# Kernel optimization log

Measured on AMD Instinct MI355X. Metric: run time of the kernel, lower is better.

The kernel has to match this reference:

```python
import jax, jax.numpy as jnp
import numpy as np

D = 1024      # n_embd
NH = 16       # attention heads
E = 8         # n_experts
K = 2         # k_best
FF = 4 * D    # expert MLP hidden
EPS = 1e-6    # rms_norm_epsilon
TEMP = 1.0    # target_temperature


def setup_inputs() -> dict:
    key = jax.random.key(0)
    ks = jax.random.split(key, 12)
    B, S = 2, 1024
    s = 0.02
    return {
        "x": jax.random.normal(ks[0], (B, S, D), jnp.float32),
        "attn_norm_w": jnp.ones((D,), jnp.float32),
        "wq": jax.random.normal(ks[1], (D, D), jnp.float32) * s,
        "wk": jax.random.normal(ks[2], (D, D), jnp.float32) * s,
        "wv": jax.random.normal(ks[3], (D, D), jnp.float32) * s,
        "wo": jax.random.normal(ks[4], (D, D), jnp.float32) * s,
        "mlp_norm_w": jnp.ones((D,), jnp.float32),
        "router_w": jax.random.normal(ks[5], (D, E), jnp.float32) * s,
        "w1": jax.random.normal(ks[6], (E, D, FF), jnp.float32) * s,
        "b1": jnp.zeros((E, FF), jnp.float32),
        "w2": jax.random.normal(ks[7], (E, FF, D), jnp.float32) * s,
        "b2": jnp.zeros((E, D), jnp.float32),
    }


def _rmsnorm(x, w):
    var = jnp.mean(jnp.square(x), axis=-1, keepdims=True)
    return x * jax.lax.rsqrt(var + EPS) * w


def _attention(x, wq, wk, wv, wo):
    B, S, _ = x.shape
    dh = D // NH
    q = (x @ wq).reshape(B, S, NH, dh)
    k = (x @ wk).reshape(B, S, NH, dh)
    v = (x @ wv).reshape(B, S, NH, dh)
    scores = jnp.einsum("bqhd,bkhd->bhqk", q, k) / jnp.sqrt(jnp.float32(dh))
    causal = jnp.tril(jnp.ones((S, S), bool))  # [S,S]
    scores = jnp.where(causal[None, None], scores, jnp.finfo(scores.dtype).min)
    attn = jax.nn.softmax(scores, axis=-1)
    out = jnp.einsum("bhqk,bkhd->bqhd", attn, v).reshape(B, S, D)
    return out @ wo


def reference(x, attn_norm_w, wq, wk, wv, wo, mlp_norm_w, router_w, w1, b1, w2, b2):
    B, S, _ = x.shape
    # attention sub-block
    x = x + _attention(_rmsnorm(x, attn_norm_w), wq, wk, wv, wo)
    residual = x
    h = _rmsnorm(x, mlp_norm_w)  # [B,S,D]

    # router: temperature softmax + top-k
    logits = h @ router_w / TEMP                      # [B,S,E]
    probs = jax.nn.softmax(logits, axis=-1)
    top_k_scores, top_k_indices = jax.lax.top_k(probs, K)  # [B,S,K]
    onehot = jax.nn.one_hot(top_k_indices, E, dtype=h.dtype)  # [B,S,K,E]
    gates = jnp.einsum("bsk,bske->bse", top_k_scores, onehot)  # [B,S,E]

    # load-balancing loss (Switch-style) + expert counts
    counts = jnp.sum(onehot, axis=(0, 1, 2))          # [E]
    frac = counts / (B * S * K)
    mean_prob = jnp.mean(probs, axis=(0, 1))          # [E]
    balancing_loss = E * jnp.sum(frac * mean_prob)

    # experts: dense dispatch; tokens with zero gate contribute nothing,
    # so this matches the sort/gather/scatter top-k combine exactly.
    pre = jnp.einsum("bsd,edf->ebsf", h, w1) + b1[:, None, None]  # [E,B,S,FF]
    act = jax.nn.gelu(pre)
    y = jnp.einsum("ebsf,efd->ebsd", act, w2) + b2[:, None, None]  # [E,B,S,D]
    moe = jnp.einsum("ebsd,bse->bsd", y, gates)

    out = residual + moe
    return out, balancing_loss, counts
```

## Files before the change

kernel.cpp:

```cpp
#include <hip/hip_runtime.h>

typedef __bf16 bf16;
typedef __bf16 bf16x4 __attribute__((ext_vector_type(4)));
typedef __bf16 bf16x8 __attribute__((ext_vector_type(8)));
typedef float f32x4 __attribute__((ext_vector_type(4)));

#define D_   1024
#define S_   1024
#define B_   2
#define NTOK 2048
#define FF_  4096
#define NE   8
#define CAP  5120
#define OUTN 2097152

__device__ __forceinline__ float gelu_f(float x) {
    float u = 0.7978845608028654f * (x + 0.044715f * x * x * x);
    float a = fabsf(u);
    float e = __expf(-2.0f * a);
    float t = (1.0f - e) / (1.0f + e);
    t = copysignf(t, u);
    return 0.5f * x * (1.0f + t);
}

__device__ __forceinline__ void gload16(const void* g, void* l) {
    __builtin_amdgcn_global_load_lds((const __attribute__((address_space(1))) unsigned int*)g,
                                     (__attribute__((address_space(3))) unsigned int*)l,
                                     16, 0, 0);
}

#define VMCNT(n) asm volatile("s_waitcnt vmcnt(" n ")" ::: "memory")
#define BARRIER() do { asm volatile("" ::: "memory"); \
                       __builtin_amdgcn_s_barrier();  \
                       asm volatile("" ::: "memory"); } while (0)

__global__ __launch_bounds__(256) void rmsnorm_k(const float* __restrict__ x,
                                                 const float* __restrict__ w,
                                                 float* __restrict__ yf,
                                                 bf16* __restrict__ yhi,
                                                 bf16* __restrict__ ylo) {
    int row = blockIdx.x;
    int t = threadIdx.x;
    const float* xr = x + (size_t)row * D_;
    float4 v = *(const float4*)(xr + t * 4);
    float ss = v.x * v.x + v.y * v.y + v.z * v.z + v.w * v.w;
    for (int off = 32; off; off >>= 1) ss += __shfl_down(ss, off);
    __shared__ float wsum[4];
    if ((t & 63) == 0) wsum[t >> 6] = ss;
    __syncthreads();
    float tot = wsum[0] + wsum[1] + wsum[2] + wsum[3];
    float rr = rsqrtf(tot * (1.0f / D_) + 1e-6f);
    float4 wv = *(const float4*)(w + t * 4);
    float y[4];
    y[0] = v.x * rr * wv.x; y[1] = v.y * rr * wv.y;
    y[2] = v.z * rr * wv.z; y[3] = v.w * rr * wv.w;
    if (yf) *(float4*)(yf + (size_t)row * D_ + t * 4) = *(float4*)y;
    if (yhi) {
#pragma unroll
        for (int i = 0; i < 4; i++) {
            bf16 hi = (bf16)y[i];
            yhi[(size_t)row * D_ + t * 4 + i] = hi;
            if (ylo) ylo[(size_t)row * D_ + t * 4 + i] = (bf16)(y[i] - (float)hi);
        }
    }
}

__global__ __launch_bounds__(256) void trans_split_k(
    const float* __restrict__ w0, const float* __restrict__ w1p,
    const float* __restrict__ w2p, const float* __restrict__ w3,
    bf16* o0h, bf16* o0l, bf16* o1h, bf16* o1l,
    bf16* o2h, bf16* o2l, bf16* o3h, bf16* o3l) {
    int z = blockIdx.z;
    const float* src = (z == 0) ? w0 : (z == 1) ? w1p : (z == 2) ? w2p : w3;
    bf16* dh = (z == 0) ? o0h : (z == 1) ? o1h : (z == 2) ? o2h : o3h;
    bf16* dl = (z == 0) ? o0l : (z == 1) ? o1l : (z == 2) ? o2l : o3l;
    __shared__ float tl[32][33];
    int c0 = blockIdx.x * 32, r0 = blockIdx.y * 32;
    int tx = threadIdx.x & 31, ty = threadIdx.x >> 5;
#pragma unroll
    for (int i = 0; i < 4; i++) {
        int r = ty + i * 8;
        tl[r][tx] = src[(size_t)(r0 + r) * 1024 + c0 + tx];
    }
    __syncthreads();
#pragma unroll
    for (int i = 0; i < 4; i++) {
        int c = ty + i * 8;
        float v = tl[tx][c];
        bf16 hi = (bf16)v;
        dh[(size_t)(c0 + c) * 1024 + r0 + tx] = hi;
        dl[(size_t)(c0 + c) * 1024 + r0 + tx] = (bf16)(v - (float)hi);
    }
}

__global__ __launch_bounds__(256) void transpose_cast4_k(const float* __restrict__ in,
                                                         bf16* __restrict__ out,
                                                         int R, int C) {
    __shared__ float tl[64][65];
    size_t base = (size_t)blockIdx.z * R * C;
    const float* src = in + base;
    bf16* dst = out + base;
    int c0 = blockIdx.x * 64, r0 = blockIdx.y * 64;
    int t = threadIdx.x;
    int lr = t >> 4;
    int lc = (t & 15) * 4;
#pragma unroll
    for (int i = 0; i < 4; i++) {
        int r = lr + i * 16;
        float4 v = *(const float4*)(src + (size_t)(r0 + r) * C + c0 + lc);
        tl[r][lc] = v.x; tl[r][lc + 1] = v.y; tl[r][lc + 2] = v.z; tl[r][lc + 3] = v.w;
    }
    __syncthreads();
    int wc = t >> 4;
    int wr = (t & 15) * 4;
#pragma unroll
    for (int i = 0; i < 4; i++) {
        int c = wc + i * 16;
        bf16x4 o;
        o[0] = (bf16)tl[wr][c];     o[1] = (bf16)tl[wr + 1][c];
        o[2] = (bf16)tl[wr + 2][c]; o[3] = (bf16)tl[wr + 3][c];
        *(bf16x4*)(dst + (size_t)(c0 + c) * R + r0 + wr) = o;
    }
}

__global__ __launch_bounds__(256) void vtrans_k(const bf16* __restrict__ vh,
                                                const bf16* __restrict__ vl,
                                                bf16* __restrict__ vth,
                                                bf16* __restrict__ vtl) {
    int s0 = blockIdx.x * 64;
    int bh = blockIdx.y;
    int b = bh >> 4, h = bh & 15;
    const bf16* src = blockIdx.z ? vl : vh;
    bf16* dst = blockIdx.z ? vtl : vth;
    __shared__ bf16 tl[64][65];
    int t = threadIdx.x;
    int lr = t >> 4, lc = (t & 15) * 4;
#pragma unroll
    for (int i = 0; i < 4; i++) {
        int r = lr + i * 16;
        bf16x4 v = *(const bf16x4*)(src + (size_t)(b * S_ + s0 + r) * D_ + h * 64 + lc);
        tl[r][lc] = v[0]; tl[r][lc + 1] = v[1]; tl[r][lc + 2] = v[2]; tl[r][lc + 3] = v[3];
    }
    __syncthreads();
    int wc = t >> 4, wr = (t & 15) * 4;
#pragma unroll
    for (int i = 0; i < 4; i++) {
        int c = wc + i * 16;
        bf16x4 o;
        o[0] = tl[wr][c];     o[1] = tl[wr + 1][c];
        o[2] = tl[wr + 2][c]; o[3] = tl[wr + 3][c];
        *(bf16x4*)(dst + (size_t)(bh * 64 + c) * S_ + s0 + wr) = o;
    }
}

#define SPLIT_STAGE(bi, k0)                             \
    gload16(gah0 + (k0), Lah[bi] + wv * 512);           \
    gload16(gah1 + (k0), Lah[bi] + 2048 + wv * 512);    \
    gload16(gal0 + (k0), Lal[bi] + wv * 512);           \
    gload16(gal1 + (k0), Lal[bi] + 2048 + wv * 512);    \
    gload16(gbh0 + (k0), Lbh[bi] + wv * 512);           \
    gload16(gbh1 + (k0), Lbh[bi] + 2048 + wv * 512);    \
    gload16(gbl0 + (k0), Lbl[bi] + wv * 512);           \
    gload16(gbl1 + (k0), Lbl[bi] + 2048 + wv * 512);

#define SPLIT_COMPUTE(bi) {                                                            \
    bf16x8 fah[4], fal[4], fbh[4], fbl[4];                                             \
    _Pragma("unroll") for (int i = 0; i < 4; i++) {                                    \
        fah[i] = *(const bf16x8*)(Lah[bi] + ra_off[i]);                                \
        fal[i] = *(const bf16x8*)(Lal[bi] + ra_off[i]);                                \
        fbh[i] = *(const bf16x8*)(Lbh[bi] + rb_off[i]);                                \
        fbl[i] = *(const bf16x8*)(Lbl[bi] + rb_off[i]);                                \
    }                                                                                  \
    _Pragma("unroll") for (int mt = 0; mt < 4; mt++)                                   \
    _Pragma("unroll") for (int nt = 0; nt < 4; nt++) {                                 \
        acc[mt][nt] = __builtin_amdgcn_mfma_f32_16x16x32_bf16(fah[mt], fbh[nt], acc[mt][nt], 0, 0, 0); \
        acc[mt][nt] = __builtin_amdgcn_mfma_f32_16x16x32_bf16(fah[mt], fbl[nt], acc[mt][nt], 0, 0, 0); \
        acc[mt][nt] = __builtin_amdgcn_mfma_f32_16x16x32_bf16(fal[mt], fbh[nt], acc[mt][nt], 0, 0, 0); \
    } }

#define SPLIT_STEP(bi, VM)          \
    VMCNT(VM);                      \
    BARRIER();                      \
    SPLIT_COMPUTE(bi);              \
    BARRIER();

#define SPLIT_DECLS(KOFF)                                                              \
    __shared__ __align__(16) bf16 Lah[2][4096];                                        \
    __shared__ __align__(16) bf16 Lal[2][4096];                                        \
    __shared__ __align__(16) bf16 Lbh[2][4096];                                        \
    __shared__ __align__(16) bf16 Lbl[2][4096];                                        \
    int t = threadIdx.x;                                                               \
    int wv = t >> 6, ln = t & 63;                                                      \
    int wm = wv >> 1, wn = wv & 1, l15 = ln & 15, qd = ln >> 4;                        \
    int sr0 = t >> 2, sr1 = 64 + sr0, cl = t & 3;                                      \
    int cs0 = (cl ^ ((sr0 >> 1) & 3)) * 8;                                             \
    int cs1 = (cl ^ ((sr1 >> 1) & 3)) * 8;                                             \
    const bf16* gah0 = Ah + (size_t)(m0 + sr0) * 1024 + (KOFF) + cs0;                  \
    const bf16* gah1 = Ah + (size_t)(m0 + sr1) * 1024 + (KOFF) + cs1;                  \
    const bf16* gal0 = Al + (size_t)(m0 + sr0) * 1024 + (KOFF) + cs0;                  \
    const bf16* gal1 = Al + (size_t)(m0 + sr1) * 1024 + (KOFF) + cs1;                  \
    const bf16* gbh0 = Bh + (size_t)(n0 + sr0) * 1024 + (KOFF) + cs0;                  \
    const bf16* gbh1 = Bh + (size_t)(n0 + sr1) * 1024 + (KOFF) + cs1;                  \
    const bf16* gbl0 = Bl + (size_t)(n0 + sr0) * 1024 + (KOFF) + cs0;                  \
    const bf16* gbl1 = Bl + (size_t)(n0 + sr1) * 1024 + (KOFF) + cs1;                  \
    int ra_off[4], rb_off[4];                                                          \
    _Pragma("unroll") for (int i = 0; i < 4; i++) {                                    \
        int r1 = wm * 64 + i * 16 + l15;                                               \
        ra_off[i] = r1 * 32 + (qd ^ ((r1 >> 1) & 3)) * 8;                              \
        int r2 = wn * 64 + i * 16 + l15;                                               \
        rb_off[i] = r2 * 32 + (qd ^ ((r2 >> 1) & 3)) * 8;                              \
    }                                                                                  \
    f32x4 acc[4][4];                                                                   \
    _Pragma("unroll") for (int mt = 0; mt < 4; mt++)                                   \
    _Pragma("unroll") for (int nt = 0; nt < 4; nt++) acc[mt][nt] = (f32x4){0.f,0.f,0.f,0.f};

__global__ __launch_bounds__(256) void gemm_qkv_k(
    const bf16* __restrict__ Ah, const bf16* __restrict__ Al,
    const bf16* __restrict__ Bqh, const bf16* __restrict__ Bql,
    const bf16* __restrict__ Bkh, const bf16* __restrict__ Bkl,
    const bf16* __restrict__ Bvh, const bf16* __restrict__ Bvl,
    bf16* Cqh, bf16* Cql, bf16* Ckh, bf16* Ckl, bf16* Cvh, bf16* Cvl) {
    int gy = blockIdx.y, zw = gy >> 3;
    const bf16* Bh = (zw == 0) ? Bqh : (zw == 1) ? Bkh : Bvh;
    const bf16* Bl = (zw == 0) ? Bql : (zw == 1) ? Bkl : Bvl;
    bf16* Ch = (zw == 0) ? Cqh : (zw == 1) ? Ckh : Cvh;
    bf16* Cl = (zw == 0) ? Cql : (zw == 1) ? Ckl : Cvl;
    int m0 = blockIdx.x * 128, n0 = (gy & 7) * 128;
    SPLIT_DECLS(0)
    SPLIT_STAGE(0, 0);
    for (int k0 = 0; k0 < 960; k0 += 64) {
        SPLIT_STAGE(1, k0 + 32);
        SPLIT_STEP(0, "8");
        SPLIT_STAGE(0, k0 + 64);
        SPLIT_STEP(1, "8");
    }
    SPLIT_STAGE(1, 992);
    SPLIT_STEP(0, "8");
    SPLIT_STEP(1, "0");
#pragma unroll
    for (int mt = 0; mt < 4; mt++)
#pragma unroll
        for (int nt = 0; nt < 4; nt++)
#pragma unroll
            for (int r = 0; r < 4; r++) {
                int gm = m0 + wm * 64 + mt * 16 + qd * 4 + r;
                int gn = n0 + wn * 64 + nt * 16 + l15;
                float vv = acc[mt][nt][r];
                bf16 hi = (bf16)vv;
                Ch[(size_t)gm * D_ + gn] = hi;
                Cl[(size_t)gm * D_ + gn] = (bf16)(vv - (float)hi);
            }
}

__global__ __launch_bounds__(256) void gemm_wo_k(
    const bf16* __restrict__ Ah, const bf16* __restrict__ Al,
    const bf16* __restrict__ Bh, const bf16* __restrict__ Bl,
    float* __restrict__ C) {
    int m0 = blockIdx.x * 128, n0 = blockIdx.y * 128;
    int kb = blockIdx.z * 256;
    SPLIT_DECLS(kb)
    SPLIT_STAGE(0, 0);
    for (int k0 = 0; k0 < 192; k0 += 64) {
        SPLIT_STAGE(1, k0 + 32);
        SPLIT_STEP(0, "8");
        SPLIT_STAGE(0, k0 + 64);
        SPLIT_STEP(1, "8");
    }
    SPLIT_STAGE(1, 224);
    SPLIT_STEP(0, "8");
    SPLIT_STEP(1, "0");
#pragma unroll
    for (int mt = 0; mt < 4; mt++)
#pragma unroll
        for (int nt = 0; nt < 4; nt++)
#pragma unroll
            for (int r = 0; r < 4; r++) {
                int gm = m0 + wm * 64 + mt * 16 + qd * 4 + r;
                int gn = n0 + wn * 64 + nt * 16 + l15;
                atomicAdd(&C[(size_t)gm * D_ + gn], acc[mt][nt][r]);
            }
}

#define AP 72

__global__ __launch_bounds__(256) void attn_mfma_k(
    const bf16* __restrict__ qhp, const bf16* __restrict__ qlp,
    const bf16* __restrict__ khp, const bf16* __restrict__ klp,
    const bf16* __restrict__ vth, const bf16* __restrict__ vtl,
    bf16* __restrict__ aoh, bf16* __restrict__ aol) {
    int qt = (int)gridDim.x - 1 - (int)blockIdx.x;
    int h = blockIdx.y, b = blockIdx.z;
    __shared__ __align__(16) bf16 Ksh[4096], Ksl[4096], VTh[4096], VTl[4096];
    __shared__ bf16 Ph[4][16 * AP], Pl[4][16 * AP];
    int t = threadIdx.x, wv = t >> 6, ln = t & 63, l15 = ln & 15, qd = ln >> 4;

    bf16x8 aqh[2], aql[2];
    {
        size_t qb = ((size_t)(b * S_ + qt * 64 + wv * 16 + l15)) * D_ + h * 64 + qd * 8;
        aqh[0] = *(const bf16x8*)(qhp + qb);
        aqh[1] = *(const bf16x8*)(qhp + qb + 32);
        aql[0] = *(const bf16x8*)(qlp + qb);
        aql[1] = *(const bf16x8*)(qlp + qb + 32);
    }

    int srow = t >> 3, scl = t & 7;
    int gsc = (scl ^ (srow & 7)) * 8;
    const bf16* kh0 = khp + (size_t)(b * S_ + srow) * D_ + h * 64 + gsc;
    const bf16* kh1 = khp + (size_t)(b * S_ + srow + 32) * D_ + h * 64 + gsc;
    const bf16* kl0 = klp + (size_t)(b * S_ + srow) * D_ + h * 64 + gsc;
    const bf16* kl1 = klp + (size_t)(b * S_ + srow + 32) * D_ + h * 64 + gsc;
    const bf16* vt0 = vth + (size_t)((b * 16 + h) * 64 + srow) * S_ + gsc;
    const bf16* vt1 = vth + (size_t)((b * 16 + h) * 64 + srow + 32) * S_ + gsc;
    const bf16* wl0 = vtl + (size_t)((b * 16 + h) * 64 + srow) * S_ + gsc;
    const bf16* wl1 = vtl + (size_t)((b * 16 + h) * 64 + srow + 32) * S_ + gsc;

    int soff[4][2];
#pragma unroll
    for (int nt = 0; nt < 4; nt++)
#pragma unroll
        for (int ks = 0; ks < 2; ks++) {
            int r = nt * 16 + l15;
            soff[nt][ks] = r * 64 + ((ks * 4 + qd) ^ (r & 7)) * 8;
        }

    f32x4 oacc[4];
    float mrow[4], lrow[4];
#pragma unroll
    for (int i = 0; i < 4; i++) {
        oacc[i] = (f32x4){0.f, 0.f, 0.f, 0.f};
        mrow[i] = -1e30f; lrow[i] = 0.0f;
    }

    for (int kt = 0; kt <= qt; kt++) {
        BARRIER();
        size_t ko = (size_t)kt * 64 * D_;
        int vo = kt * 64;
        gload16(kh0 + ko, Ksh + wv * 512); gload16(kh1 + ko, Ksh + 2048 + wv * 512);
        gload16(kl0 + ko, Ksl + wv * 512); gload16(kl1 + ko, Ksl + 2048 + wv * 512);
        gload16(vt0 + vo, VTh + wv * 512); gload16(vt1 + vo, VTh + 2048 + wv * 512);
        gload16(wl0 + vo, VTl + wv * 512); gload16(wl1 + vo, VTl + 2048 + wv * 512);
        VMCNT("0");
        BARRIER();

        f32x4 sacc[4];
#pragma unroll
        for (int nt = 0; nt < 4; nt++) sacc[nt] = (f32x4){0.f, 0.f, 0.f, 0.f};
#pragma unroll
        for (int ks = 0; ks < 2; ks++) {
#pragma unroll
            for (int nt = 0; nt < 4; nt++) {
                bf16x8 bh = *(const bf16x8*)&Ksh[soff[nt][ks]];
                bf16x8 bl = *(const bf16x8*)&Ksl[soff[nt][ks]];
                sacc[nt] = __builtin_amdgcn_mfma_f32_16x16x32_bf16(aqh[ks], bh, sacc[nt], 0, 0, 0);
                sacc[nt] = __builtin_amdgcn_mfma_f32_16x16x32_bf16(aqh[ks], bl, sacc[nt], 0, 0, 0);
                sacc[nt] = __builtin_amdgcn_mfma_f32_16x16x32_bf16(aql[ks], bh, sacc[nt], 0, 0, 0);
            }
        }
        bool diag = (kt == qt);
#pragma unroll
        for (int r = 0; r < 4; r++) {
            float s0[4];
#pragma unroll
            for (int nt = 0; nt < 4; nt++) {
                s0[nt] = sacc[nt][r] * 0.125f;
                if (diag && (nt * 16 + l15) > (wv * 16 + qd * 4 + r)) s0[nt] = -1e30f;
            }
            float vmax = fmaxf(fmaxf(s0[0], s0[1]), fmaxf(s0[2], s0[3]));
            for (int off = 1; off < 16; off <<= 1) vmax = fmaxf(vmax, __shfl_xor(vmax, off));
            float mnew = fmaxf(mrow[r], vmax);
            float alpha = __expf(mrow[r] - mnew);
            float p[4], rs = 0.0f;
#pragma unroll
            for (int nt = 0; nt < 4; nt++) { p[nt] = __expf(s0[nt] - mnew); rs += p[nt]; }
            for (int off = 1; off < 16; off <<= 1) rs += __shfl_xor(rs, off);
            lrow[r] = lrow[r] * alpha + rs;
            mrow[r] = mnew;
#pragma unroll
            for (int nt = 0; nt < 4; nt++) oacc[nt][r] *= alpha;
            int prow = qd * 4 + r;
#pragma unroll
            for (int nt = 0; nt < 4; nt++) {
                bf16 hi = (bf16)p[nt];
                Ph[wv][prow * AP + nt * 16 + l15] = hi;
                Pl[wv][prow * AP + nt * 16 + l15] = (bf16)(p[nt] - (float)hi);
            }
        }
#pragma unroll
        for (int ks2 = 0; ks2 < 2; ks2++) {
            bf16x8 aph = *(const bf16x8*)&Ph[wv][l15 * AP + ks2 * 32 + qd * 8];
            bf16x8 apl = *(const bf16x8*)&Pl[wv][l15 * AP + ks2 * 32 + qd * 8];
#pragma unroll
            for (int nt = 0; nt < 4; nt++) {
                bf16x8 bvh = *(const bf16x8*)&VTh[soff[nt][ks2]];
                bf16x8 bvl = *(const bf16x8*)&VTl[soff[nt][ks2]];
                oacc[nt] = __builtin_amdgcn_mfma_f32_16x16x32_bf16(aph, bvh, oacc[nt], 0, 0, 0);
                oacc[nt] = __builtin_amdgcn_mfma_f32_16x16x32_bf16(aph, bvl, oacc[nt], 0, 0, 0);
                oacc[nt] = __builtin_amdgcn_mfma_f32_16x16x32_bf16(apl, bvh, oacc[nt], 0, 0, 0);
            }
        }
    }

#pragma unroll
    for (int r = 0; r < 4; r++) {
        float inv = 1.0f / lrow[r];
        size_t rowa = ((size_t)(b * S_ + qt * 64 + wv * 16 + qd * 4 + r)) * D_ + h * 64;
#pragma unroll
        for (int nt = 0; nt < 4; nt++) {
            float o = oacc[nt][r] * inv;
            bf16 hi = (bf16)o;
            aoh[rowa + nt * 16 + l15] = hi;
            aol[rowa + nt * 16 + l15] = (bf16)(o - (float)hi);
        }
    }
}

__global__ __launch_bounds__(256) void router_k(const float* __restrict__ h,
                                                const float* __restrict__ rw,
                                                int* __restrict__ tidx,
                                                float* __restrict__ tgate,
                                                int* __restrict__ ecnt,
                                                float* __restrict__ psum) {
    int wv = threadIdx.x >> 6, ln = threadIdx.x & 63;
    int tok = blockIdx.x * 4 + wv;
    const float* hr = h + (size_t)tok * D_;
    float acc[NE];
#pragma unroll
    for (int e = 0; e < NE; e++) acc[e] = 0.0f;
    int base = ln * 16;
#pragma unroll
    for (int c = 0; c < 4; c++) {
        float4 hv = *(const float4*)(hr + base + c * 4);
        const float* rp = rw + (size_t)(base + c * 4) * NE;
        float hx[4] = {hv.x, hv.y, hv.z, hv.w};
#pragma unroll
        for (int jj = 0; jj < 4; jj++)
#pragma unroll
            for (int e = 0; e < NE; e++)
                acc[e] = fmaf(hx[jj], rp[jj * NE + e], acc[e]);
    }
#pragma unroll
    for (int e = 0; e < NE; e++)
        for (int off = 32; off; off >>= 1) acc[e] += __shfl_down(acc[e], off);

    __shared__ float pb[4][NE];
    if (ln == 0) {
        float mx = acc[0];
#pragma unroll
        for (int e = 1; e < NE; e++) mx = fmaxf(mx, acc[e]);
        float p[NE], ssum = 0.0f;
#pragma unroll
        for (int e = 0; e < NE; e++) { p[e] = expf(acc[e] - mx); ssum += p[e]; }
        float inv = 1.0f / ssum;
#pragma unroll
        for (int e = 0; e < NE; e++) p[e] *= inv;
        int i0 = 0; float b0 = p[0];
#pragma unroll
        for (int e = 1; e < NE; e++) if (p[e] > b0) { b0 = p[e]; i0 = e; }
        int i1 = -1; float b1v = -1.0f;
#pragma unroll
        for (int e = 0; e < NE; e++) if (e != i0 && p[e] > b1v) { b1v = p[e]; i1 = e; }
        tidx[tok * 2] = i0; tidx[tok * 2 + 1] = i1;
        tgate[tok * 2] = b0; tgate[tok * 2 + 1] = b1v;
        atomicAdd(&ecnt[i0], 1);
        atomicAdd(&ecnt[i1], 1);
#pragma unroll
        for (int e = 0; e < NE; e++) pb[wv][e] = p[e];
    }
    __syncthreads();
    if (threadIdx.x < NE) {
        float s2 = pb[0][threadIdx.x] + pb[1][threadIdx.x] + pb[2][threadIdx.x] + pb[3][threadIdx.x];
        atomicAdd(&psum[threadIdx.x], s2);
    }
}

__global__ void passb_k(const int* __restrict__ ecnt, const float* __restrict__ psum,
                        int* __restrict__ eoffp, int* __restrict__ ecnt2,
                        float* __restrict__ out_tail) {
    if (threadIdx.x == 0) {
        int off = 0; float loss = 0.0f;
        for (int e = 0; e < NE; e++) {
            eoffp[e] = off;
            int c = ecnt[e];
            off += (c + 127) & ~127;
            loss += (c * (1.0f / 4096.0f)) * (psum[e] * (1.0f / 2048.0f));
            out_tail[1 + e] = (float)c;
            ecnt2[e] = 0;
        }
        eoffp[NE] = off;
        out_tail[0] = 8.0f * loss;
    }
}

__global__ __launch_bounds__(256) void scatter_k(const int* __restrict__ tidx,
                                                 const int* __restrict__ eoffp,
                                                 int* __restrict__ ecnt2,
                                                 int* __restrict__ stok,
                                                 int* __restrict__ sidx) {
    int tok = blockIdx.x * 256 + threadIdx.x;
    for (int k = 0; k < 2; k++) {
        int e = tidx[tok * 2 + k];
        int pos = eoffp[e] + atomicAdd(&ecnt2[e], 1);
        stok[pos] = tok;
        sidx[tok * 2 + k] = pos;
    }
}

#define MOE_STAGE(bufA, bufB, k0)                       \
    gload16(ga0 + (k0), (bufA) + wv * 512);             \
    gload16(ga1 + (k0), (bufA) + 2048 + wv * 512);      \
    gload16(gb0 + (k0), (bufB) + wv * 512);             \
    gload16(gb1 + (k0), (bufB) + 2048 + wv * 512);

#define MOE_TILE(bufA, bufB) {                                                         \
    bf16x8 af[4], bfr[4];                                                              \
    _Pragma("unroll") for (int i = 0; i < 4; i++) {                                    \
        af[i]  = *(const bf16x8*)((bufA) + ra_off[i]);                                 \
        bfr[i] = *(const bf16x8*)((bufB) + rb_off[i]);                                 \
    }                                                                                  \
    _Pragma("unroll") for (int mt = 0; mt < 4; mt++)                                   \
    _Pragma("unroll") for (int nt = 0; nt < 4; nt++)                                   \
        acc[mt][nt] = __builtin_amdgcn_mfma_f32_16x16x32_bf16(af[mt], bfr[nt], acc[mt][nt], 0, 0, 0); }

#define MOE_STEP(rdA, rdB, VM)      \
    VMCNT(VM);                      \
    BARRIER();                      \
    MOE_TILE(rdA, rdB);             \
    BARRIER();

__global__ __launch_bounds__(256) void moe_gemm1_k(const bf16* __restrict__ hB,
                                                   const bf16* __restrict__ w1t,
                                                   const float* __restrict__ b1,
                                                   const int* __restrict__ eoffp,
                                                   const int* __restrict__ stok,
                                                   bf16* __restrict__ act) {
    int m0 = blockIdx.x * 128, n0 = blockIdx.y * 128;
    if (m0 >= eoffp[NE]) return;
    int e = 0;
#pragma unroll
    for (int i = 1; i < NE; i++) if (m0 >= eoffp[i]) e = i;

    __shared__ __align__(16) bf16 As[2][4096];
    __shared__ __align__(16) bf16 Bs[2][4096];
    int t = threadIdx.x;
    int wv = t >> 6, ln = t & 63;
    int wm = wv >> 1, wn = wv & 1, l15 = ln & 15, qd = ln >> 4;

    int sr0 = t >> 2, sr1 = 64 + sr0, cl = t & 3;
    int cs0 = (cl ^ ((sr0 >> 1) & 3)) * 8;
    int cs1 = (cl ^ ((sr1 >> 1) & 3)) * 8;
    const bf16* ga0 = hB + (size_t)stok[m0 + sr0] * D_ + cs0;
    const bf16* ga1 = hB + (size_t)stok[m0 + sr1] * D_ + cs1;
    const bf16* Bb = w1t + ((size_t)e * FF_ + n0) * D_;
    const bf16* gb0 = Bb + (size_t)sr0 * D_ + cs0;
    const bf16* gb1 = Bb + (size_t)sr1 * D_ + cs1;

    int ra_off[4], rb_off[4];
#pragma unroll
    for (int i = 0; i < 4; i++) {
        int r1 = wm * 64 + i * 16 + l15;
        ra_off[i] = r1 * 32 + (qd ^ ((r1 >> 1) & 3)) * 8;
        int r2 = wn * 64 + i * 16 + l15;
        rb_off[i] = r2 * 32 + (qd ^ ((r2 >> 1) & 3)) * 8;
    }

    f32x4 acc[4][4];
#pragma unroll
    for (int mt = 0; mt < 4; mt++)
#pragma unroll
        for (int nt = 0; nt < 4; nt++) acc[mt][nt] = (f32x4){0.f, 0.f, 0.f, 0.f};

    MOE_STAGE(As[0], Bs[0], 0);
    for (int k0 = 0; k0 < 960; k0 += 64) {
        MOE_STAGE(As[1], Bs[1], k0 + 32);
        MOE_STEP(As[0], Bs[0], "4");
        MOE_STAGE(As[0], Bs[0], k0 + 64);
        MOE_STEP(As[1], Bs[1], "4");
    }
    MOE_STAGE(As[1], Bs[1], 992);
    MOE_STEP(As[0], Bs[0], "4");
    MOE_STEP(As[1], Bs[1], "0");

    const float* b1e = b1 + (size_t)e * FF_;
#pragma unroll
    for (int mt = 0; mt < 4; mt++)
#pragma unroll
        for (int nt = 0; nt < 4; nt++) {
            int gn = n0 + wn * 64 + nt * 16 + l15;
            float bias = b1e[gn];
#pragma unroll
            for (int r = 0; r < 4; r++) {
                int gm = m0 + wm * 64 + mt * 16 + qd * 4 + r;
                act[(size_t)gm * FF_ + gn] = (bf16)gelu_f(acc[mt][nt][r] + bias);
            }
        }
}

__global__ __launch_bounds__(256) void moe_gemm2_k(const bf16* __restrict__ act,
                                                   const bf16* __restrict__ w2t,
                                                   const float* __restrict__ b2,
                                                   const int* __restrict__ eoffp,
                                                   float* __restrict__ y) {
    int m0 = blockIdx.x * 128, n0 = blockIdx.y * 128;
    if (m0 >= eoffp[NE]) return;
    int e = 0;
#pragma unroll
    for (int i = 1; i < NE; i++) if (m0 >= eoffp[i]) e = i;

    __shared__ __align__(16) bf16 As[4][4096];
    __shared__ __align__(16) bf16 Bs[4][4096];
    int t = threadIdx.x;
    int wv = t >> 6, ln = t & 63;
    int wm = wv >> 1, wn = wv & 1, l15 = ln & 15, qd = ln >> 4;

    int sr0 = t >> 2, sr1 = 64 + sr0, cl = t & 3;
    int cs0 = (cl ^ ((sr0 >> 1) & 3)) * 8;
    int cs1 = (cl ^ ((sr1 >> 1) & 3)) * 8;
    const bf16* ga0 = act + (size_t)(m0 + sr0) * FF_ + cs0;
    const bf16* ga1 = act + (size_t)(m0 + sr1) * FF_ + cs1;
    const bf16* Bb = w2t + ((size_t)e * D_ + n0) * FF_;
    const bf16* gb0 = Bb + (size_t)sr0 * FF_ + cs0;
    const bf16* gb1 = Bb + (size_t)sr1 * FF_ + cs1;

    int ra_off[4], rb_off[4];
#pragma unroll
    for (int i = 0; i < 4; i++) {
        int r1 = wm * 64 + i * 16 + l15;
        ra_off[i] = r1 * 32 + (qd ^ ((r1 >> 1) & 3)) * 8;
        int r2 = wn * 64 + i * 16 + l15;
        rb_off[i] = r2 * 32 + (qd ^ ((r2 >> 1) & 3)) * 8;
    }

    f32x4 acc[4][4];
#pragma unroll
    for (int mt = 0; mt < 4; mt++)
#pragma unroll
        for (int nt = 0; nt < 4; nt++) acc[mt][nt] = (f32x4){0.f, 0.f, 0.f, 0.f};

    MOE_STAGE(As[0], Bs[0], 0);
    MOE_STAGE(As[1], Bs[1], 32);
    for (int k0 = 0; k0 < 3968; k0 += 128) {
        MOE_STAGE(As[2], Bs[2], k0 + 64);  MOE_STEP(As[0], Bs[0], "8");
        MOE_STAGE(As[3], Bs[3], k0 + 96);  MOE_STEP(As[1], Bs[1], "8");
        MOE_STAGE(As[0], Bs[0], k0 + 128); MOE_STEP(As[2], Bs[2], "8");
        MOE_STAGE(As[1], Bs[1], k0 + 160); MOE_STEP(As[3], Bs[3], "8");
    }
    MOE_STAGE(As[2], Bs[2], 4032); MOE_STEP(As[0], Bs[0], "8");
    MOE_STAGE(As[3], Bs[3], 4064); MOE_STEP(As[1], Bs[1], "8");
    MOE_STEP(As[2], Bs[2], "4");
    MOE_STEP(As[3], Bs[3], "0");

    const float* b2e = b2 + (size_t)e * D_;
#pragma unroll
    for (int mt = 0; mt < 4; mt++)
#pragma unroll
        for (int nt = 0; nt < 4; nt++) {
            int gn = n0 + wn * 64 + nt * 16 + l15;
            float bias = b2e[gn];
#pragma unroll
            for (int r = 0; r < 4; r++) {
                int gm = m0 + wm * 64 + mt * 16 + qd * 4 + r;
                y[(size_t)gm * D_ + gn] = acc[mt][nt][r] + bias;
            }
        }
}

__global__ __launch_bounds__(256) void combine_k(const float* __restrict__ y,
                                                 const int* __restrict__ sidx,
                                                 const float* __restrict__ tgate,
                                                 float* __restrict__ out) {
    int tok = blockIdx.x;
    int d = threadIdx.x * 4;
    int s0 = sidx[tok * 2], s1 = sidx[tok * 2 + 1];
    float g0 = tgate[tok * 2], g1 = tgate[tok * 2 + 1];
    float4 a = *(const float4*)(y + (size_t)s0 * D_ + d);
    float4 b = *(const float4*)(y + (size_t)s1 * D_ + d);
    float4 o = *(const float4*)(out + (size_t)tok * D_ + d);
    o.x += g0 * a.x + g1 * b.x;
    o.y += g0 * a.y + g1 * b.y;
    o.z += g0 * a.z + g1 * b.z;
    o.w += g0 * a.w + g1 * b.w;
    *(float4*)(out + (size_t)tok * D_ + d) = o;
}

extern "C" void kernel_launch(void* const* d_in, const int* in_sizes, int n_in,
                              void* d_out, int out_size, void* d_ws, size_t ws_size,
                              hipStream_t stream) {
    const float* x   = (const float*)d_in[0];
    const float* anw = (const float*)d_in[1];
    const float* wq  = (const float*)d_in[2];
    const float* wk  = (const float*)d_in[3];
    const float* wv  = (const float*)d_in[4];
    const float* wo  = (const float*)d_in[5];
    const float* mnw = (const float*)d_in[6];
    const float* rw  = (const float*)d_in[7];
    const float* w1  = (const float*)d_in[8];
    const float* b1  = (const float*)d_in[9];
    const float* w2  = (const float*)d_in[10];
    const float* b2  = (const float*)d_in[11];
    float* out = (float*)d_out;

    char* p = (char*)d_ws;
    auto take = [&](size_t n) { char* r = p; p += (n + 255) & ~(size_t)255; return r; };
    bf16* h1h = (bf16*)take((size_t)OUTN * 2);
    bf16* h1l = (bf16*)take((size_t)OUTN * 2);
    bf16* qh  = (bf16*)take((size_t)OUTN * 2);
    bf16* ql  = (bf16*)take((size_t)OUTN * 2);
    bf16* kh  = (bf16*)take((size_t)OUTN * 2);
    bf16* kl  = (bf16*)take((size_t)OUTN * 2);
    bf16* vh  = (bf16*)take((size_t)OUTN * 2);
    bf16* vl  = (bf16*)take((size_t)OUTN * 2);
    bf16* vth = (bf16*)take((size_t)OUTN * 2);
    bf16* vtl = (bf16*)take((size_t)OUTN * 2);
    bf16* wqth = (bf16*)take((size_t)D_ * D_ * 2);
    bf16* wqtl = (bf16*)take((size_t)D_ * D_ * 2);
    bf16* wkth = (bf16*)take((size_t)D_ * D_ * 2);
    bf16* wktl = (bf16*)take((size_t)D_ * D_ * 2);
    bf16* wvth = (bf16*)take((size_t)D_ * D_ * 2);
    bf16* wvtl = (bf16*)take((size_t)D_ * D_ * 2);
    bf16* woth = (bf16*)take((size_t)D_ * D_ * 2);
    bf16* wotl = (bf16*)take((size_t)D_ * D_ * 2);
    bf16* w1t = (bf16*)take((size_t)NE * FF_ * D_ * 2);
    bf16* w2t = (bf16*)take((size_t)NE * FF_ * D_ * 2);
    bf16* act = (bf16*)take((size_t)CAP * FF_ * 2);
    int*   tidx  = (int*)take(NTOK * 2 * 4);
    float* tgate = (float*)take(NTOK * 2 * 4);
    int*   sidx  = (int*)take(NTOK * 2 * 4);
    int*   ecnt  = (int*)take(64);
    int*   ecnt2 = (int*)take(64);
    float* psum  = (float*)take(64);
    int*   eoffp = (int*)take(64);
    int*   stok  = (int*)take(CAP * 4);

    bf16*  aoh = h1h;
    bf16*  aol = h1l;
    float* h_f = (float*)qh;
    bf16*  h_b = kh;
    float* y   = (float*)vh;

    hipMemsetAsync(ecnt, 0, NE * 4, stream);
    hipMemsetAsync(psum, 0, NE * 4, stream);
    hipMemsetAsync(stok, 0, CAP * 4, stream);
    hipMemcpyAsync(out, x, (size_t)OUTN * 4, hipMemcpyDeviceToDevice, stream);

    trans_split_k<<<dim3(32, 32, 4), 256, 0, stream>>>(wq, wk, wv, wo,
        wqth, wqtl, wkth, wktl, wvth, wvtl, woth, wotl);
    transpose_cast4_k<<<dim3(FF_ / 64, D_ / 64, NE), 256, 0, stream>>>(w1, w1t, D_, FF_);
    transpose_cast4_k<<<dim3(D_ / 64, FF_ / 64, NE), 256, 0, stream>>>(w2, w2t, FF_, D_);

    rmsnorm_k<<<NTOK, 256, 0, stream>>>(x, anw, nullptr, h1h, h1l);
    gemm_qkv_k<<<dim3(16, 24), 256, 0, stream>>>(h1h, h1l,
        wqth, wqtl, wkth, wktl, wvth, wvtl, qh, ql, kh, kl, vh, vl);
    vtrans_k<<<dim3(S_ / 64, 32, 2), 256, 0, stream>>>(vh, vl, vth, vtl);
    attn_mfma_k<<<dim3(16, 16, 2), 256, 0, stream>>>(qh, ql, kh, kl, vth, vtl, aoh, aol);
    gemm_wo_k<<<dim3(16, 8, 4), 256, 0, stream>>>(aoh, aol, woth, wotl, out);

    rmsnorm_k<<<NTOK, 256, 0, stream>>>(out, mnw, h_f, h_b, nullptr);
    router_k<<<NTOK / 4, 256, 0, stream>>>(h_f, rw, tidx, tgate, ecnt, psum);
    passb_k<<<1, 64, 0, stream>>>(ecnt, psum, eoffp, ecnt2, out + OUTN);
    scatter_k<<<NTOK / 256, 256, 0, stream>>>(tidx, eoffp, ecnt2, stok, sidx);
    moe_gemm1_k<<<dim3(CAP / 128, FF_ / 128), 256, 0, stream>>>(h_b, w1t, b1, eoffp, stok, act);
    moe_gemm2_k<<<dim3(CAP / 128, D_ / 128), 256, 0, stream>>>(act, w2t, b2, eoffp, y);
    combine_k<<<NTOK, 256, 0, stream>>>(y, sidx, tgate, out);
}
```

Before: 742.3 us.

## Enlarge MoE GEMM tiles to 256x256 with 512 threads and split-K for second GEMM

```diff
diff --git a/kernel.cpp b/kernel.cpp
--- a/kernel.cpp
+++ b/kernel.cpp
@@ -11,7 +11,7 @@
 #define NTOK 2048
 #define FF_  4096
 #define NE   8
-#define CAP  5120
+#define CAP  6144
 #define OUTN 2097152
 
 __device__ __forceinline__ float gelu_f(float x) {
@@ -481,7 +481,7 @@
         for (int e = 0; e < NE; e++) {
             eoffp[e] = off;
             int c = ecnt[e];
-            off += (c + 127) & ~127;
+            off += (c + 255) & ~255;
             loss += (c * (1.0f / 4096.0f)) * (psum[e] * (1.0f / 2048.0f));
             out_tail[1 + e] = (float)c;
             ecnt2[e] = 0;
@@ -505,161 +505,143 @@
     }
 }
 
-#define MOE_STAGE(bufA, bufB, k0)                       \
+#define MOE2_STAGE(bufA, bufB, k0)                      \
     gload16(ga0 + (k0), (bufA) + wv * 512);             \
-    gload16(ga1 + (k0), (bufA) + 2048 + wv * 512);      \
+    gload16(ga1 + (k0), (bufA) + 4096 + wv * 512);      \
     gload16(gb0 + (k0), (bufB) + wv * 512);             \
-    gload16(gb1 + (k0), (bufB) + 2048 + wv * 512);
-
-#define MOE_TILE(bufA, bufB) {                                                         \
-    bf16x8 af[4], bfr[4];                                                              \
-    _Pragma("unroll") for (int i = 0; i < 4; i++) {                                    \
-        af[i]  = *(const bf16x8*)((bufA) + ra_off[i]);                                 \
+    gload16(gb1 + (k0), (bufB) + 4096 + wv * 512);
+
+#define MOE2_TILE(bufA, bufB) {                                                        \
+    bf16x8 af[8], bfr[4];                                                              \
+    _Pragma("unroll") for (int i = 0; i < 8; i++)                                      \
+        af[i] = *(const bf16x8*)((bufA) + ra_off[i]);                                  \
+    _Pragma("unroll") for (int i = 0; i < 4; i++)                                      \
         bfr[i] = *(const bf16x8*)((bufB) + rb_off[i]);                                 \
-    }                                                                                  \
-    _Pragma("unroll") for (int mt = 0; mt < 4; mt++)                                   \
+    _Pragma("unroll") for (int mt = 0; mt < 8; mt++)                                   \
     _Pragma("unroll") for (int nt = 0; nt < 4; nt++)                                   \
         acc[mt][nt] = __builtin_amdgcn_mfma_f32_16x16x32_bf16(af[mt], bfr[nt], acc[mt][nt], 0, 0, 0); }
 
-#define MOE_STEP(rdA, rdB, VM)      \
+#define MOE2_STEP(rdA, rdB, VM)     \
     VMCNT(VM);                      \
     BARRIER();                      \
-    MOE_TILE(rdA, rdB);             \
+    MOE2_TILE(rdA, rdB);            \
     BARRIER();
 
-__global__ __launch_bounds__(256) void moe_gemm1_k(const bf16* __restrict__ hB,
+#define MOE2_DECLS                                                                     \
+    int t = threadIdx.x;                                                               \
+    int wv = t >> 6, ln = t & 63;                                                      \
+    int wm = wv >> 2, wn = wv & 3, l15 = ln & 15, qd = ln >> 4;                        \
+    int sr0 = t >> 2, sr1 = 128 + sr0, cl = t & 3;                                     \
+    int cs0 = (cl ^ ((sr0 >> 1) & 3)) * 8;                                             \
+    int cs1 = (cl ^ ((sr1 >> 1) & 3)) * 8;                                             \
+    int ra_off[8], rb_off[4];                                                          \
+    _Pragma("unroll") for (int i = 0; i < 8; i++) {                                    \
+        int r1 = wm * 128 + i * 16 + l15;                                              \
+        ra_off[i] = r1 * 32 + (qd ^ ((r1 >> 1) & 3)) * 8;                              \
+    }                                                                                  \
+    _Pragma("unroll") for (int i = 0; i < 4; i++) {                                    \
+        int r2 = wn * 64 + i * 16 + l15;                                               \
+        rb_off[i] = r2 * 32 + (qd ^ ((r2 >> 1) & 3)) * 8;                              \
+    }                                                                                  \
+    f32x4 acc[8][4];                                                                   \
+    _Pragma("unroll") for (int mt = 0; mt < 8; mt++)                                   \
+    _Pragma("unroll") for (int nt = 0; nt < 4; nt++) acc[mt][nt] = (f32x4){0.f,0.f,0.f,0.f};
+
+__global__ __launch_bounds__(512) void moe_gemm1_k(const bf16* __restrict__ hB,
                                                    const bf16* __restrict__ w1t,
                                                    const float* __restrict__ b1,
                                                    const int* __restrict__ eoffp,
                                                    const int* __restrict__ stok,
                                                    bf16* __restrict__ act) {
-    int m0 = blockIdx.x * 128, n0 = blockIdx.y * 128;
+    int m0 = blockIdx.x * 256, n0 = blockIdx.y * 256;
     if (m0 >= eoffp[NE]) return;
     int e = 0;
 #pragma unroll
     for (int i = 1; i < NE; i++) if (m0 >= eoffp[i]) e = i;
 
-    __shared__ __align__(16) bf16 As[2][4096];
-    __shared__ __align__(16) bf16 Bs[2][4096];
-    int t = threadIdx.x;
-    int wv = t >> 6, ln = t & 63;
-    int wm = wv >> 1, wn = wv & 1, l15 = ln & 15, qd = ln >> 4;
-
-    int sr0 = t >> 2, sr1 = 64 + sr0, cl = t & 3;
-    int cs0 = (cl ^ ((sr0 >> 1) & 3)) * 8;
-    int cs1 = (cl ^ ((sr1 >> 1) & 3)) * 8;
+    __shared__ __align__(16) bf16 As[2][8192];
+    __shared__ __align__(16) bf16 Bs[2][8192];
+    MOE2_DECLS
+
     const bf16* ga0 = hB + (size_t)stok[m0 + sr0] * D_ + cs0;
     const bf16* ga1 = hB + (size_t)stok[m0 + sr1] * D_ + cs1;
     const bf16* Bb = w1t + ((size_t)e * FF_ + n0) * D_;
     const bf16* gb0 = Bb + (size_t)sr0 * D_ + cs0;
     const bf16* gb1 = Bb + (size_t)sr1 * D_ + cs1;
 
-    int ra_off[4], rb_off[4];
-#pragma unroll
-    for (int i = 0; i < 4; i++) {
-        int r1 = wm * 64 + i * 16 + l15;
-        ra_off[i] = r1 * 32 + (qd ^ ((r1 >> 1) & 3)) * 8;
-        int r2 = wn * 64 + i * 16 + l15;
-        rb_off[i] = r2 * 32 + (qd ^ ((r2 >> 1) & 3)) * 8;
-    }
-
-    f32x4 acc[4][4];
-#pragma unroll
-    for (int mt = 0; mt < 4; mt++)
-#pragma unroll
-        for (int nt = 0; nt < 4; nt++) acc[mt][nt] = (f32x4){0.f, 0.f, 0.f, 0.f};
-
-    MOE_STAGE(As[0], Bs[0], 0);
+    MOE2_STAGE(As[0], Bs[0], 0);
     for (int k0 = 0; k0 < 960; k0 += 64) {
-        MOE_STAGE(As[1], Bs[1], k0 + 32);
-        MOE_STEP(As[0], Bs[0], "4");
-        MOE_STAGE(As[0], Bs[0], k0 + 64);
-        MOE_STEP(As[1], Bs[1], "4");
-    }
-    MOE_STAGE(As[1], Bs[1], 992);
-    MOE_STEP(As[0], Bs[0], "4");
-    MOE_STEP(As[1], Bs[1], "0");
+        MOE2_STAGE(As[1], Bs[1], k0 + 32);
+        MOE2_STEP(As[0], Bs[0], "4");
+        MOE2_STAGE(As[0], Bs[0], k0 + 64);
+        MOE2_STEP(As[1], Bs[1], "4");
+    }
+    MOE2_STAGE(As[1], Bs[1], 992);
+    MOE2_STEP(As[0], Bs[0], "4");
+    MOE2_STEP(As[1], Bs[1], "0");
 
     const float* b1e = b1 + (size_t)e * FF_;
 #pragma unroll
-    for (int mt = 0; mt < 4; mt++)
+    for (int mt = 0; mt < 8; mt++)
 #pragma unroll
         for (int nt = 0; nt < 4; nt++) {
             int gn = n0 + wn * 64 + nt * 16 + l15;
             float bias = b1e[gn];
 #pragma unroll
             for (int r = 0; r < 4; r++) {
-                int gm = m0 + wm * 64 + mt * 16 + qd * 4 + r;
+                int gm = m0 + wm * 128 + mt * 16 + qd * 4 + r;
                 act[(size_t)gm * FF_ + gn] = (bf16)gelu_f(acc[mt][nt][r] + bias);
             }
         }
 }
 
-__global__ __launch_bounds__(256) void moe_gemm2_k(const bf16* __restrict__ act,
+__global__ __launch_bounds__(512) void moe_gemm2_k(const bf16* __restrict__ act,
                                                    const bf16* __restrict__ w2t,
                                                    const float* __restrict__ b2,
                                                    const int* __restrict__ eoffp,
                                                    float* __restrict__ y) {
-    int m0 = blockIdx.x * 128, n0 = blockIdx.y * 128;
+    int m0 = blockIdx.x * 256, n0 = blockIdx.y * 256;
     if (m0 >= eoffp[NE]) return;
     int e = 0;
 #pragma unroll
     for (int i = 1; i < NE; i++) if (m0 >= eoffp[i]) e = i;
-
-    __shared__ __align__(16) bf16 As[4][4096];
-    __shared__ __align__(16) bf16 Bs[4][4096];
-    int t = threadIdx.x;
-    int wv = t >> 6, ln = t & 63;
-    int wm = wv >> 1, wn = wv & 1, l15 = ln & 15, qd = ln >> 4;
-
-    int sr0 = t >> 2, sr1 = 64 + sr0, cl = t & 3;
-    int cs0 = (cl ^ ((sr0 >> 1) & 3)) * 8;
-    int cs1 = (cl ^ ((sr1 >> 1) & 3)) * 8;
-    const bf16* ga0 = act + (size_t)(m0 + sr0) * FF_ + cs0;
-    const bf16* ga1 = act + (size_t)(m0 + sr1) * FF_ + cs1;
+    int zk = blockIdx.z;
+    int kbase = zk * 2048;
+
+    __shared__ __align__(16) bf16 As[4][8192];
+    __shared__ __align__(16) bf16 Bs[4][8192];
+    MOE2_DECLS
+
+    const bf16* ga0 = act + (size_t)(m0 + sr0) * FF_ + kbase + cs0;
+    const bf16* ga1 = act + (size_t)(m0 + sr1) * FF_ + kbase + cs1;
     const bf16* Bb = w2t + ((size_t)e * D_ + n0) * FF_;
-    const bf16* gb0 = Bb + (size_t)sr0 * FF_ + cs0;
-    const bf16* gb1 = Bb + (size_t)sr1 * FF_ + cs1;
-
-    int ra_off[4], rb_off[4];
-#pragma unroll
-    for (int i = 0; i < 4; i++) {
-        int r1 = wm * 64 + i * 16 + l15;
-        ra_off[i] = r1 * 32 + (qd ^ ((r1 >> 1) & 3)) * 8;
-        int r2 = wn * 64 + i * 16 + l15;
-        rb_off[i] = r2 * 32 + (qd ^ ((r2 >> 1) & 3)) * 8;
-    }
-
-    f32x4 acc[4][4];
-#pragma unroll
-    for (int mt = 0; mt < 4; mt++)
-#pragma unroll
-        for (int nt = 0; nt < 4; nt++) acc[mt][nt] = (f32x4){0.f, 0.f, 0.f, 0.f};
-
-    MOE_STAGE(As[0], Bs[0], 0);
-    MOE_STAGE(As[1], Bs[1], 32);
-    for (int k0 = 0; k0 < 3968; k0 += 128) {
-        MOE_STAGE(As[2], Bs[2], k0 + 64);  MOE_STEP(As[0], Bs[0], "8");
-        MOE_STAGE(As[3], Bs[3], k0 + 96);  MOE_STEP(As[1], Bs[1], "8");
-        MOE_STAGE(As[0], Bs[0], k0 + 128); MOE_STEP(As[2], Bs[2], "8");
-        MOE_STAGE(As[1], Bs[1], k0 + 160); MOE_STEP(As[3], Bs[3], "8");
-    }
-    MOE_STAGE(As[2], Bs[2], 4032); MOE_STEP(As[0], Bs[0], "8");
-    MOE_STAGE(As[3], Bs[3], 4064); MOE_STEP(As[1], Bs[1], "8");
-    MOE_STEP(As[2], Bs[2], "4");
-    MOE_STEP(As[3], Bs[3], "0");
+    const bf16* gb0 = Bb + (size_t)sr0 * FF_ + kbase + cs0;
+    const bf16* gb1 = Bb + (size_t)sr1 * FF_ + kbase + cs1;
+
+    MOE2_STAGE(As[0], Bs[0], 0);
+    MOE2_STAGE(As[1], Bs[1], 32);
+    for (int k0 = 0; k0 < 1920; k0 += 128) {
+        MOE2_STAGE(As[2], Bs[2], k0 + 64);  MOE2_STEP(As[0], Bs[0], "8");
+        MOE2_STAGE(As[3], Bs[3], k0 + 96);  MOE2_STEP(As[1], Bs[1], "8");
+        MOE2_STAGE(As[0], Bs[0], k0 + 128); MOE2_STEP(As[2], Bs[2], "8");
+        MOE2_STAGE(As[1], Bs[1], k0 + 160); MOE2_STEP(As[3], Bs[3], "8");
+    }
+    MOE2_STAGE(As[2], Bs[2], 1984); MOE2_STEP(As[0], Bs[0], "8");
+    MOE2_STAGE(As[3], Bs[3], 2016); MOE2_STEP(As[1], Bs[1], "8");
+    MOE2_STEP(As[2], Bs[2], "4");
+    MOE2_STEP(As[3], Bs[3], "0");
 
     const float* b2e = b2 + (size_t)e * D_;
 #pragma unroll
-    for (int mt = 0; mt < 4; mt++)
+    for (int mt = 0; mt < 8; mt++)
 #pragma unroll
         for (int nt = 0; nt < 4; nt++) {
             int gn = n0 + wn * 64 + nt * 16 + l15;
-            float bias = b2e[gn];
+            float bias = (zk == 0) ? b2e[gn] : 0.0f;
 #pragma unroll
             for (int r = 0; r < 4; r++) {
-                int gm = m0 + wm * 64 + mt * 16 + qd * 4 + r;
-                y[(size_t)gm * D_ + gn] = acc[mt][nt][r] + bias;
+                int gm = m0 + wm * 128 + mt * 16 + qd * 4 + r;
+                atomicAdd(&y[(size_t)gm * D_ + gn], acc[mt][nt][r] + bias);
             }
         }
 }
@@ -754,11 +736,12 @@
     attn_mfma_k<<<dim3(16, 16, 2), 256, 0, stream>>>(qh, ql, kh, kl, vth, vtl, aoh, aol);
     gemm_wo_k<<<dim3(16, 8, 4), 256, 0, stream>>>(aoh, aol, woth, wotl, out);
 
+    hipMemsetAsync(y, 0, (size_t)CAP * D_ * 4, stream);
     rmsnorm_k<<<NTOK, 256, 0, stream>>>(out, mnw, h_f, h_b, nullptr);
     router_k<<<NTOK / 4, 256, 0, stream>>>(h_f, rw, tidx, tgate, ecnt, psum);
     passb_k<<<1, 64, 0, stream>>>(ecnt, psum, eoffp, ecnt2, out + OUTN);
     scatter_k<<<NTOK / 256, 256, 0, stream>>>(tidx, eoffp, ecnt2, stok, sidx);
-    moe_gemm1_k<<<dim3(CAP / 128, FF_ / 128), 256, 0, stream>>>(h_b, w1t, b1, eoffp, stok, act);
-    moe_gemm2_k<<<dim3(CAP / 128, D_ / 128), 256, 0, stream>>>(act, w2t, b2, eoffp, y);
+    moe_gemm1_k<<<dim3(CAP / 256, FF_ / 256), 512, 0, stream>>>(h_b, w1t, b1, eoffp, stok, act);
+    moe_gemm2_k<<<dim3(CAP / 256, D_ / 256, 2), 512, 0, stream>>>(act, w2t, b2, eoffp, y);
     combine_k<<<NTOK, 256, 0, stream>>>(y, sidx, tgate, out);
 }
```

After: 762.3 us. +2.7%, slower.
